# Optimization experiments

Hardware: AMD Instinct MI355X
Metric: run time of the kernel (lower is better)

The kernel has to match this reference:

```python
import jax, jax.numpy as jnp
import numpy as np

B, S, D = 4, 4096, 2048
K, H = 64, 32
HD = K // H  # 2
LN_EPS = 1e-5


def setup_inputs() -> dict:
    key = jax.random.key(0)
    ks = jax.random.split(key, 8)
    def xavier(k, shape):
        fan_in, fan_out = shape[1], shape[0]
        lim = float(np.sqrt(6.0 / (fan_in + fan_out)))
        return jax.random.uniform(k, shape, jnp.float32, -lim, lim)
    return {
        "x": jax.random.normal(ks[0], (B, S, D), jnp.float32),
        "norm_w": jnp.ones((D,), jnp.float32),
        "norm_b": jnp.zeros((D,), jnp.float32),
        "qkv_w": xavier(ks[1], (3 * K, D)),
        "qkv_b": jnp.zeros((3 * K,), jnp.float32),
        "fm_w": xavier(ks[2], (HD, HD)),
        "fm_b": jnp.zeros((HD,), jnp.float32),
        "out_w": xavier(ks[3], (D, K)),
        "out_b": jnp.zeros((D,), jnp.float32),
    }


def reference(x, norm_w, norm_b, qkv_w, qkv_b, fm_w, fm_b, out_w, out_b):
    # LayerNorm
    mu = jnp.mean(x, axis=-1, keepdims=True)
    var = jnp.var(x, axis=-1, keepdims=True)
    xn = (x - mu) * jax.lax.rsqrt(var + LN_EPS) * norm_w + norm_b
    # QKV projection: [B,S,3K]
    qkv = xn @ qkv_w.T + qkv_b
    q, k, v = jnp.split(qkv, 3, axis=-1)
    # [B,S,K] -> [B,H,S,hd]
    def heads(t):
        return t.reshape(B, S, H, HD).transpose(0, 2, 1, 3)
    q, k, v = heads(q), heads(k), heads(v)
    # feature map: ReLU(Linear)
    q = jax.nn.relu(q @ fm_w.T + fm_b)
    k = jax.nn.relu(k @ fm_w.T + fm_b)
    # linear attention: kv state [B,H,hd,hd]
    kv = jnp.einsum('bhsd,bhse->bhde', k, v)
    attn = jnp.einsum('bhsd,bhde->bhse', q, kv)
    k_sum = jnp.sum(k, axis=2)                      # [B,H,hd]
    q_k_sum = jnp.einsum('bhsd,bhd->bhs', q, k_sum)[..., None]
    attn = attn / (q_k_sum + 1e-8)
    # merge heads -> [B,S,K]
    attn = attn.transpose(0, 2, 1, 3).reshape(B, S, K)
    out = attn @ out_w.T + out_b
    return x + out
```

## Files before the change

### kernel.cpp

```cpp
#include <hip/hip_runtime.h>
#include <hip/hip_bf16.h>
#include <stdint.h>

typedef unsigned short ushort_t;

#define BB 4
#define SS 4096
#define DD 2048
#define KKC 64
#define HH 32
#define NT (BB*SS)
#define NQKV 192
#define QB 64

typedef float f32x4 __attribute__((ext_vector_type(4)));
typedef short s16x8 __attribute__((ext_vector_type(8)));

__device__ __forceinline__ ushort_t f2bf(float f) {
    union { float f; uint32_t u; } c; c.f = f;
    uint32_t u = c.u + 0x7fffu + ((c.u >> 16) & 1u);
    return (ushort_t)(u >> 16);
}
__device__ __forceinline__ float bf2f(ushort_t b) {
    union { uint32_t u; float f; } c; c.u = (uint32_t)b << 16; return c.f;
}

__device__ __forceinline__ uint32_t cvtpk(float lo, float hi) {
    uint32_t r;
    asm("v_cvt_pk_bf16_f32 %0, %1, %2" : "=v"(r) : "v"(lo), "v"(hi));
    return r;
}

__device__ __forceinline__ void mfma16(f32x4& d, s16x8 a, s16x8 b) {
    asm volatile("v_mfma_f32_16x16x32_bf16 %0, %1, %2, %0" : "+v"(d) : "v"(a), "v"(b));
}

__global__ __launch_bounds__(256) void k_pre(
    const float* __restrict__ qkv_w, const float* __restrict__ nw,
    const float* __restrict__ nb, const float* __restrict__ qkv_b,
    const float* __restrict__ out_w,
    ushort_t* __restrict__ W1, ushort_t* __restrict__ W2,
    float* __restrict__ S, float* __restrict__ qb2) {
    int bid = blockIdx.x;
    if (bid < 256) {
        int E = bid * 256 + threadIdx.x;
        if (E < 49152) {
            int lane = E & 63; int rest = E >> 6;
            int f = rest % 12, g = rest / 12;
            int col = f * 16 + (lane & 15);
            int k0 = g * 32 + 8 * (lane >> 4);
            const float* src = qkv_w + (size_t)col * DD + k0;
            const float* wp = nw + k0;
            union { ushort_t u[8]; uint4 v; } cv;
            #pragma unroll
            for (int e = 0; e < 8; ++e) cv.u[e] = f2bf(src[e] * wp[e]);
            *(uint4*)(W1 + (size_t)E * 8) = cv.v;
        } else {
            int E2 = E - 49152;
            int lane = E2 & 63; int rest = E2 >> 6;
            int kk = rest & 1, F = rest >> 1;
            int n = F * 16 + (lane & 15);
            int k0 = kk * 32 + 8 * (lane >> 4);
            const float* src = out_w + (size_t)n * KKC + k0;
            union { ushort_t u[8]; uint4 v; } cv;
            #pragma unroll
            for (int e = 0; e < 8; ++e) cv.u[e] = f2bf(src[e]);
            *(uint4*)(W2 + (size_t)E2 * 8) = cv.v;
        }
    } else {
        int col = (bid - 256) * 4 + (threadIdx.x >> 6);
        int lane = threadIdx.x & 63;
        float s = 0.f, qb = 0.f;
        for (int j = 0; j < 32; ++j) {
            int k = j * 64 + lane;
            float w = qkv_w[(size_t)col * DD + k];
            s += bf2f(f2bf(w * nw[k]));
            qb += nb[k] * w;
        }
        #pragma unroll
        for (int off = 32; off >= 1; off >>= 1) {
            s += __shfl_xor(s, off);
            qb += __shfl_xor(qb, off);
        }
        if (lane == 0) { S[col] = s; qb2[col] = qb + qkv_b[col]; }
    }
}

__global__ __launch_bounds__(512, 2) void k_qkv(
    const float* __restrict__ x, const ushort_t* __restrict__ W1,
    const float* __restrict__ S, const float* __restrict__ qb2,
    const float* __restrict__ fm_w, const float* __restrict__ fm_b,
    float* __restrict__ qfeat,
    float* __restrict__ kvpart)
{
    __shared__ __align__(16) union {
        ushort_t xb[8][2][16][64];
        float cep[QB][NQKV];
    } sm;
    __shared__ float kvred[32][16][6];
    __shared__ float stats[QB][2];

    const int tid = threadIdx.x;
    const int wave = tid >> 6, lane = tid & 63;
    const int rg = wave & 3, ch = wave >> 2;
    const int m0 = blockIdx.x * QB;
    const int fbase = ch * 6;
    const int l15 = lane & 15, q4 = lane >> 4;
    const bool doStats = (ch == 0);

    const float* xbase = x + (size_t)(m0 + rg * 16 + q4) * DD + l15 * 4;
    int wb[4];
    #pragma unroll
    for (int i = 0; i < 4; ++i) {
        int r = i * 4 + q4;
        wb[i] = r * 128 + ((l15 >> 1) ^ (r & 7)) * 16 + (l15 & 1) * 8;
    }
    const s16x8* __restrict__ Wp = (const s16x8*)W1;

    f32x4 acc[6];
    #pragma unroll
    for (int j = 0; j < 6; ++j) acc[j] = (f32x4){0.f, 0.f, 0.f, 0.f};
    float st1[4] = {0.f, 0.f, 0.f, 0.f}, st2[4] = {0.f, 0.f, 0.f, 0.f};

#define LOADX(T, X) do { \
        _Pragma("unroll") \
        for (int i_ = 0; i_ < 4; ++i_) \
            X[i_] = *(const float4*)(xbase + (size_t)(i_ * 4) * DD + (T) * 64); \
    } while (0)

#define LOADB(T, D) do { \
        _Pragma("unroll") \
        for (int kb_ = 0; kb_ < 2; ++kb_) \
        { _Pragma("unroll") \
          for (int cf_ = 0; cf_ < 6; ++cf_) \
            D[kb_][cf_] = Wp[((size_t)(2 * (T) + kb_) * 12 + fbase + cf_) * 64 + lane]; } \
    } while (0)

#define CVTW(T, X) do { \
        char* xbw_ = (char*)&sm.xb[wave][(T) & 1][0][0]; \
        _Pragma("unroll") \
        for (int i_ = 0; i_ < 4; ++i_) { \
            if (doStats) { \
                st1[i_] += X[i_].x + X[i_].y + X[i_].z + X[i_].w; \
                st2[i_] += X[i_].x*X[i_].x + X[i_].y*X[i_].y \
                         + X[i_].z*X[i_].z + X[i_].w*X[i_].w; \
            } \
            uint2 w_; \
            w_.x = cvtpk(X[i_].x, X[i_].y); \
            w_.y = cvtpk(X[i_].z, X[i_].w); \
            *(uint2*)(xbw_ + wb[i_]) = w_; \
        } \
    } while (0)

#define AREAD(T, AF) do { \
        const char* xbr_ = (const char*)&sm.xb[wave][(T) & 1][0][0]; \
        _Pragma("unroll") \
        for (int kb_ = 0; kb_ < 2; ++kb_) \
            AF[kb_] = *(const s16x8*)(xbr_ + l15 * 128 + (((kb_ * 4 + q4) ^ (l15 & 7)) << 4)); \
    } while (0)

#define MM(AF, D) do { \
        _Pragma("unroll") \
        for (int kb_ = 0; kb_ < 2; ++kb_) \
        { _Pragma("unroll") \
          for (int cf_ = 0; cf_ < 6; ++cf_) \
            mfma16(acc[cf_], AF[kb_], D[kb_][cf_]); } \
    } while (0)

    float4 xA[4], xB[4];
    s16x8 Ba[2][6], Bb[2][6], af[2];

    LOADX(0, xA);
    LOADB(0, Ba);
    CVTW(0, xA);

    for (int tp = 0; tp < 16; ++tp) {
        const int t0 = 2 * tp, t1 = t0 + 1;
        LOADX(t1, xB); LOADB(t1, Bb);
        AREAD(t0, af); MM(af, Ba);
        CVTW(t1, xB);
        if (t1 < 31) { LOADX(t1 + 1, xA); LOADB(t1 + 1, Ba); }
        AREAD(t1, af); MM(af, Bb);
        if (t1 < 31) CVTW(t1 + 1, xA);
    }
#undef LOADX
#undef LOADB
#undef CVTW
#undef AREAD
#undef MM

    if (doStats) {
        #pragma unroll
        for (int i = 0; i < 4; ++i) {
            float s1 = st1[i], s2 = st2[i];
            s1 += __shfl_xor(s1, 1); s2 += __shfl_xor(s2, 1);
            s1 += __shfl_xor(s1, 2); s2 += __shfl_xor(s2, 2);
            s1 += __shfl_xor(s1, 4); s2 += __shfl_xor(s2, 4);
            s1 += __shfl_xor(s1, 8); s2 += __shfl_xor(s2, 8);
            if (l15 == 0) {
                int row = rg * 16 + i * 4 + q4;
                float mu = s1 * (1.f / DD);
                float var = s2 * (1.f / DD) - mu * mu;
                stats[row][0] = mu;
                stats[row][1] = rsqrtf(var + 1e-5f);
            }
        }
    }
    __syncthreads();

    #pragma unroll
    for (int j = 0; j < 6; ++j) {
        int col = (fbase + j) * 16 + l15;
        int rbase = rg * 16 + q4 * 4;
        #pragma unroll
        for (int r = 0; r < 4; ++r)
            sm.cep[rbase + r][col] = acc[j][r];
    }
    __syncthreads();

    const int h = tid & 31, gg = tid >> 5;
    const float fm00 = fm_w[0], fm01 = fm_w[1], fm10 = fm_w[2], fm11 = fm_w[3];
    const float fb0 = fm_b[0], fb1 = fm_b[1];
    const float Sq0 = S[2*h],      Sq1 = S[2*h+1],      cq0 = qb2[2*h],      cq1 = qb2[2*h+1];
    const float Sk0 = S[64+2*h],   Sk1 = S[64+2*h+1],   ck0 = qb2[64+2*h],   ck1 = qb2[64+2*h+1];
    const float Sv0 = S[128+2*h],  Sv1 = S[128+2*h+1],  cv0 = qb2[128+2*h],  cv1 = qb2[128+2*h+1];
    float kv00=0, kv01=0, kv10=0, kv11=0, ks0=0, ks1=0;
    #pragma unroll
    for (int i = 0; i < 4; ++i) {
        int tt = gg * 4 + i;
        float mu = stats[tt][0], rs = stats[tt][1];
        float f = mu * rs;
        float q0 = rs * sm.cep[tt][2*h]      - f * Sq0 + cq0;
        float q1 = rs * sm.cep[tt][2*h+1]    - f * Sq1 + cq1;
        float k0 = rs * sm.cep[tt][64+2*h]   - f * Sk0 + ck0;
        float k1 = rs * sm.cep[tt][64+2*h+1] - f * Sk1 + ck1;
        float v0 = rs * sm.cep[tt][128+2*h]  - f * Sv0 + cv0;
        float v1 = rs * sm.cep[tt][128+2*h+1]- f * Sv1 + cv1;
        float qp0 = fmaxf(fm00*q0 + fm01*q1 + fb0, 0.f);
        float qp1 = fmaxf(fm10*q0 + fm11*q1 + fb1, 0.f);
        float kp0 = fmaxf(fm00*k0 + fm01*k1 + fb0, 0.f);
        float kp1 = fmaxf(fm10*k0 + fm11*k1 + fb1, 0.f);
        *(float2*)(qfeat + (size_t)(m0 + tt) * KKC + 2*h) = make_float2(qp0, qp1);
        kv00 += kp0*v0; kv01 += kp0*v1; kv10 += kp1*v0; kv11 += kp1*v1;
        ks0 += kp0; ks1 += kp1;
    }
    kvred[h][gg][0]=kv00; kvred[h][gg][1]=kv01; kvred[h][gg][2]=kv10;
    kvred[h][gg][3]=kv11; kvred[h][gg][4]=ks0;  kvred[h][gg][5]=ks1;
    __syncthreads();
    if (tid < 192) {
        int h2 = tid / 6, j = tid % 6;
        float s = 0.f;
        #pragma unroll
        for (int g2 = 0; g2 < 16; ++g2) s += kvred[h2][g2][j];
        kvpart[(size_t)blockIdx.x * 192 + tid] = s;
    }
}

#define CEP_STRIDE 260
__global__ __launch_bounds__(512, 4) void k_out(
    const float* __restrict__ qfeat, const float* __restrict__ kvpart,
    const ushort_t* __restrict__ W2, const float* __restrict__ out_b,
    const float* __restrict__ x, float* __restrict__ out) {
    __shared__ float skv[192];
    __shared__ __align__(16) float cep[32 * CEP_STRIDE];
    const int tid = threadIdx.x, wave = tid >> 6, lane = tid & 63;
    const int rg = wave & 1, cq = wave >> 1;
    const int mb = blockIdx.x >> 1, nb = blockIdx.x & 1;
    const int m0 = mb * 32;
    const int n0 = nb * 1024;
    const int b = m0 >> 12;

    if (tid < 192) {
        float s = 0.f;
        #pragma unroll 8
        for (int j = 0; j < 64; ++j)
            s += kvpart[(size_t)(b * 64 + j) * 192 + tid];
        skv[tid] = s;
    }

    const int arow = m0 + rg * 16 + (lane & 15);
    const int ksub = 8 * (lane >> 4);
    float4 qa0 = *(const float4*)(qfeat + (size_t)arow * KKC + ksub);
    float4 qa1 = *(const float4*)(qfeat + (size_t)arow * KKC + ksub + 4);
    float4 qb0 = *(const float4*)(qfeat + (size_t)arow * KKC + 32 + ksub);
    float4 qb1 = *(const float4*)(qfeat + (size_t)arow * KKC + 32 + ksub + 4);
    __syncthreads();

    union { ushort_t u[8]; s16x8 v; } ca, cb;
    {
        float qs[8] = {qa0.x,qa0.y,qa0.z,qa0.w,qa1.x,qa1.y,qa1.z,qa1.w};
        float rs[8] = {qb0.x,qb0.y,qb0.z,qb0.w,qb1.x,qb1.y,qb1.z,qb1.w};
        #pragma unroll
        for (int e = 0; e < 8; e += 2) {
            int h = (ksub + e) >> 1;
            const float* kv = skv + h * 6;
            float q0 = qs[e], q1 = qs[e+1];
            float inv = 1.f / (q0 * kv[4] + q1 * kv[5] + 1e-8f);
            ca.u[e]   = f2bf((q0 * kv[0] + q1 * kv[2]) * inv);
            ca.u[e+1] = f2bf((q0 * kv[1] + q1 * kv[3]) * inv);
            const float* kw = skv + (h + 16) * 6;
            float p0 = rs[e], p1 = rs[e+1];
            float iw = 1.f / (p0 * kw[4] + p1 * kw[5] + 1e-8f);
            cb.u[e]   = f2bf((p0 * kw[0] + p1 * kw[2]) * iw);
            cb.u[e+1] = f2bf((p0 * kw[1] + p1 * kw[3]) * iw);
        }
    }

    f32x4 acc[16];
    #pragma unroll
    for (int j = 0; j < 16; ++j) acc[j] = (f32x4){0.f, 0.f, 0.f, 0.f};
    #pragma unroll
    for (int j = 0; j < 16; ++j) {
        int Fg = (n0 >> 4) + cq + 4 * j;
        s16x8 b0 = *(const s16x8*)(W2 + ((size_t)(Fg * 2 + 0) * 64 + lane) * 8);
        s16x8 b1 = *(const s16x8*)(W2 + ((size_t)(Fg * 2 + 1) * 64 + lane) * 8);
        mfma16(acc[j], ca.v, b0);
        mfma16(acc[j], cb.v, b1);
    }

    const int wrow = rg * 16 + 4 * (lane >> 4);
    #pragma unroll
    for (int n = 0; n < 4; ++n) {
        #pragma unroll
        for (int i = 0; i < 4; ++i) {
            int col = cq * 16 + i * 64 + (lane & 15);
            #pragma unroll
            for (int r = 0; r < 4; ++r)
                cep[(wrow + r) * CEP_STRIDE + col] = acc[4 * n + i][r];
        }
        __syncthreads();
        #pragma unroll
        for (int p = 0; p < 4; ++p) {
            int row = p * 8 + (tid >> 6);
            int c4 = tid & 63;
            float4 c = *(const float4*)(cep + row * CEP_STRIDE + c4 * 4);
            int gcol = n0 + n * 256 + c4 * 4;
            size_t off = (size_t)(m0 + row) * DD + gcol;
            float4 xr = *(const float4*)(x + off);
            float4 ob = *(const float4*)(out_b + gcol);
            float4 o;
            o.x = c.x + ob.x + xr.x; o.y = c.y + ob.y + xr.y;
            o.z = c.z + ob.z + xr.z; o.w = c.w + ob.w + xr.w;
            *(float4*)(out + off) = o;
        }
        __syncthreads();
    }
}

extern "C" void kernel_launch(void* const* d_in, const int* in_sizes, int n_in,
                              void* d_out, int out_size, void* d_ws, size_t ws_size,
                              hipStream_t stream) {
    const float* x     = (const float*)d_in[0];
    const float* nw    = (const float*)d_in[1];
    const float* nb    = (const float*)d_in[2];
    const float* qkv_w = (const float*)d_in[3];
    const float* qkv_b = (const float*)d_in[4];
    const float* fm_w  = (const float*)d_in[5];
    const float* fm_b  = (const float*)d_in[6];
    const float* out_w = (const float*)d_in[7];
    const float* out_b = (const float*)d_in[8];
    float* out = (float*)d_out;

    char* ws = (char*)d_ws;
    ushort_t* W1 = (ushort_t*)ws;     ws += (size_t)NQKV * DD * 2;
    ushort_t* W2 = (ushort_t*)ws;     ws += (size_t)DD * KKC * 2;
    float* qfeat = (float*)ws;        ws += (size_t)NT * KKC * 4;
    float* kvpart = (float*)ws;       ws += (size_t)256 * 192 * 4;
    float* Svec = (float*)ws;         ws += (size_t)NQKV * 4;
    float* qb2 = (float*)ws;          ws += (size_t)NQKV * 4;

    k_pre<<<304, 256, 0, stream>>>(qkv_w, nw, nb, qkv_b, out_w, W1, W2, Svec, qb2);
    k_qkv<<<NT / QB, 512, 0, stream>>>(x, W1, Svec, qb2, fm_w, fm_b, qfeat, kvpart);
    k_out<<<(NT / 32) * 2, 512, 0, stream>>>(qfeat, kvpart, W2, out_b, x, out);
}
```

Before: 121.2 us.

## Stage QKV weights via global_load_lds with BK=128 double buffering; add kv reduce kernel

The QKV GEMM main loop is restructured. The block loads a 64x128 x tile cooperatively and converts it to bf16 into swizzled LDS. The pre-packed W1 tiles are staged straight into LDS with global_load_lds, double-buffered, using explicit waitcnt/barrier control and setprio around the MFMAs. Each wave now computes 32 rows by 3 column fragments instead of 16 rows by 6, so B operands are shared through LDS rather than loaded per wave from global. Separately, a tiny k_red kernel reduces the kvpart sums once, so every k_out block no longer repeats the 64-way reduction. This adds one kernel launch and larger LDS usage, which may lower occupancy.

After: 119.3 us. Within noise of the previous version (-1.6%).

```diff
diff --git a/kernel.cpp b/kernel.cpp
--- a/kernel.cpp
+++ b/kernel.cpp
@@ -12,6 +12,7 @@
 #define NT (BB*SS)
 #define NQKV 192
 #define QB 64
+#define BK 128
 
 typedef float f32x4 __attribute__((ext_vector_type(4)));
 typedef short s16x8 __attribute__((ext_vector_type(8)));
@@ -33,6 +34,13 @@
 
 __device__ __forceinline__ void mfma16(f32x4& d, s16x8 a, s16x8 b) {
     asm volatile("v_mfma_f32_16x16x32_bf16 %0, %1, %2, %0" : "+v"(d) : "v"(a), "v"(b));
+}
+
+__device__ __forceinline__ void gload_lds16(const void* gsrc, void* ldst) {
+    __builtin_amdgcn_global_load_lds(
+        (const __attribute__((address_space(1))) unsigned int*)gsrc,
+        (__attribute__((address_space(3))) unsigned int*)ldst,
+        16, 0, 0);
 }
 
 __global__ __launch_bounds__(256) void k_pre(
@@ -94,7 +102,12 @@
     float* __restrict__ kvpart)
 {
     __shared__ __align__(16) union {
-        ushort_t xb[8][2][16][64];
+        struct {
+            ushort_t B0[3072 * 8];
+            ushort_t X0[QB * BK];
+            ushort_t B1[3072 * 8];
+            ushort_t X1[QB * BK];
+        } s;
         float cep[QB][NQKV];
     } sm;
     __shared__ float kvred[32][16][6];
@@ -102,119 +115,137 @@
 
     const int tid = threadIdx.x;
     const int wave = tid >> 6, lane = tid & 63;
-    const int rg = wave & 3, ch = wave >> 2;
+    const int rg = wave & 1, ch = wave >> 1;
     const int m0 = blockIdx.x * QB;
-    const int fbase = ch * 6;
     const int l15 = lane & 15, q4 = lane >> 4;
-    const bool doStats = (ch == 0);
-
-    const float* xbase = x + (size_t)(m0 + rg * 16 + q4) * DD + l15 * 4;
-    int wb[4];
-    #pragma unroll
-    for (int i = 0; i < 4; ++i) {
-        int r = i * 4 + q4;
-        wb[i] = r * 128 + ((l15 >> 1) ^ (r & 7)) * 16 + (l15 & 1) * 8;
-    }
-    const s16x8* __restrict__ Wp = (const s16x8*)W1;
-
-    f32x4 acc[6];
-    #pragma unroll
-    for (int j = 0; j < 6; ++j) acc[j] = (f32x4){0.f, 0.f, 0.f, 0.f};
-    float st1[4] = {0.f, 0.f, 0.f, 0.f}, st2[4] = {0.f, 0.f, 0.f, 0.f};
-
-#define LOADX(T, X) do { \
+
+    const int row0 = tid >> 4;
+    const int sl0 = tid & 15;
+    const int row1 = row0 + 32;
+    const float* xs0 = x + (size_t)(m0 + row0) * DD + sl0 * 8;
+    const float* xs1 = x + (size_t)(m0 + row1) * DD + sl0 * 8;
+    const int wb0 = row0 * 256 + ((sl0 ^ (row0 & 7)) << 4);
+    const int wb1 = row1 * 256 + ((sl0 ^ (row1 & 7)) << 4);
+
+    f32x4 acc[2][3];
+    #pragma unroll
+    for (int rf = 0; rf < 2; ++rf)
+        #pragma unroll
+        for (int f = 0; f < 3; ++f) acc[rf][f] = (f32x4){0.f, 0.f, 0.f, 0.f};
+    float st1[2] = {0.f, 0.f}, st2[2] = {0.f, 0.f};
+
+    float4 xa[4];
+
+#define XISSUE(T) do { \
+        xa[0] = *(const float4*)(xs0 + (size_t)(T) * BK); \
+        xa[1] = *(const float4*)(xs0 + (size_t)(T) * BK + 4); \
+        xa[2] = *(const float4*)(xs1 + (size_t)(T) * BK); \
+        xa[3] = *(const float4*)(xs1 + (size_t)(T) * BK + 4); \
+    } while (0)
+
+#define BSTAGE(T, BARR) do { \
         _Pragma("unroll") \
-        for (int i_ = 0; i_ < 4; ++i_) \
-            X[i_] = *(const float4*)(xbase + (size_t)(i_ * 4) * DD + (T) * 64); \
-    } while (0)
-
-#define LOADB(T, D) do { \
-        _Pragma("unroll") \
-        for (int kb_ = 0; kb_ < 2; ++kb_) \
-        { _Pragma("unroll") \
-          for (int cf_ = 0; cf_ < 6; ++cf_) \
-            D[kb_][cf_] = Wp[((size_t)(2 * (T) + kb_) * 12 + fbase + cf_) * 64 + lane]; } \
-    } while (0)
-
-#define CVTW(T, X) do { \
-        char* xbw_ = (char*)&sm.xb[wave][(T) & 1][0][0]; \
-        _Pragma("unroll") \
-        for (int i_ = 0; i_ < 4; ++i_) { \
-            if (doStats) { \
-                st1[i_] += X[i_].x + X[i_].y + X[i_].z + X[i_].w; \
-                st2[i_] += X[i_].x*X[i_].x + X[i_].y*X[i_].y \
-                         + X[i_].z*X[i_].z + X[i_].w*X[i_].w; \
-            } \
-            uint2 w_; \
-            w_.x = cvtpk(X[i_].x, X[i_].y); \
-            w_.y = cvtpk(X[i_].z, X[i_].w); \
-            *(uint2*)(xbw_ + wb[i_]) = w_; \
+        for (int i_ = 0; i_ < 6; ++i_) { \
+            int eb_ = i_ * 512 + wave * 64; \
+            gload_lds16((const char*)W1 + ((size_t)(T) * 3072 + eb_ + lane) * 16, \
+                        (char*)(BARR) + eb_ * 16); \
         } \
     } while (0)
 
-#define AREAD(T, AF) do { \
-        const char* xbr_ = (const char*)&sm.xb[wave][(T) & 1][0][0]; \
+#define CVTW(XARR) do { \
+        st1[0] += xa[0].x+xa[0].y+xa[0].z+xa[0].w + xa[1].x+xa[1].y+xa[1].z+xa[1].w; \
+        st2[0] += xa[0].x*xa[0].x+xa[0].y*xa[0].y+xa[0].z*xa[0].z+xa[0].w*xa[0].w \
+                + xa[1].x*xa[1].x+xa[1].y*xa[1].y+xa[1].z*xa[1].z+xa[1].w*xa[1].w; \
+        st1[1] += xa[2].x+xa[2].y+xa[2].z+xa[2].w + xa[3].x+xa[3].y+xa[3].z+xa[3].w; \
+        st2[1] += xa[2].x*xa[2].x+xa[2].y*xa[2].y+xa[2].z*xa[2].z+xa[2].w*xa[2].w \
+                + xa[3].x*xa[3].x+xa[3].y*xa[3].y+xa[3].z*xa[3].z+xa[3].w*xa[3].w; \
+        uint4 w0_, w1_; \
+        w0_.x = cvtpk(xa[0].x, xa[0].y); w0_.y = cvtpk(xa[0].z, xa[0].w); \
+        w0_.z = cvtpk(xa[1].x, xa[1].y); w0_.w = cvtpk(xa[1].z, xa[1].w); \
+        w1_.x = cvtpk(xa[2].x, xa[2].y); w1_.y = cvtpk(xa[2].z, xa[2].w); \
+        w1_.z = cvtpk(xa[3].x, xa[3].y); w1_.w = cvtpk(xa[3].z, xa[3].w); \
+        *(uint4*)((char*)(XARR) + wb0) = w0_; \
+        *(uint4*)((char*)(XARR) + wb1) = w1_; \
+    } while (0)
+
+#define STEP_BODY(BARR, XARR) do { \
+        const char* bp_ = (const char*)(BARR); \
+        const char* xp_ = (const char*)(XARR); \
+        const int r0_ = rg * 32 + l15, r1_ = r0_ + 16; \
         _Pragma("unroll") \
-        for (int kb_ = 0; kb_ < 2; ++kb_) \
-            AF[kb_] = *(const s16x8*)(xbr_ + l15 * 128 + (((kb_ * 4 + q4) ^ (l15 & 7)) << 4)); \
+        for (int kb_ = 0; kb_ < 4; ++kb_) { \
+            s16x8 a0_ = *(const s16x8*)(xp_ + r0_ * 256 + (((kb_ * 4 + q4) ^ (r0_ & 7)) << 4)); \
+            s16x8 a1_ = *(const s16x8*)(xp_ + r1_ * 256 + (((kb_ * 4 + q4) ^ (r1_ & 7)) << 4)); \
+            __builtin_amdgcn_s_setprio(1); \
+            _Pragma("unroll") \
+            for (int f_ = 0; f_ < 3; ++f_) { \
+                s16x8 b_ = *(const s16x8*)(bp_ + ((kb_ * 12 + ch * 3 + f_) * 64 + lane) * 16); \
+                mfma16(acc[0][f_], a0_, b_); \
+                mfma16(acc[1][f_], a1_, b_); \
+            } \
+            __builtin_amdgcn_s_setprio(0); \
+        } \
     } while (0)
 
-#define MM(AF, D) do { \
-        _Pragma("unroll") \
-        for (int kb_ = 0; kb_ < 2; ++kb_) \
-        { _Pragma("unroll") \
-          for (int cf_ = 0; cf_ < 6; ++cf_) \
-            mfma16(acc[cf_], AF[kb_], D[kb_][cf_]); } \
+#define WAITN(N) asm volatile("s_waitcnt vmcnt(" #N ")" ::: "memory")
+#define LGKM0()  asm volatile("s_waitcnt lgkmcnt(0)" ::: "memory")
+#define BARR_()  do { __builtin_amdgcn_s_barrier(); __builtin_amdgcn_sched_barrier(0); } while (0)
+
+#define ITER(T, CB, CX, NB_, NX_) do { \
+        XISSUE((T) + 1); \
+        BSTAGE((T) + 1, NB_); \
+        STEP_BODY(CB, CX); \
+        WAITN(6); \
+        CVTW(NX_); \
+        LGKM0(); \
+        WAITN(0); \
+        BARR_(); \
     } while (0)
 
-    float4 xA[4], xB[4];
-    s16x8 Ba[2][6], Bb[2][6], af[2];
-
-    LOADX(0, xA);
-    LOADB(0, Ba);
-    CVTW(0, xA);
-
-    for (int tp = 0; tp < 16; ++tp) {
-        const int t0 = 2 * tp, t1 = t0 + 1;
-        LOADX(t1, xB); LOADB(t1, Bb);
-        AREAD(t0, af); MM(af, Ba);
-        CVTW(t1, xB);
-        if (t1 < 31) { LOADX(t1 + 1, xA); LOADB(t1 + 1, Ba); }
-        AREAD(t1, af); MM(af, Bb);
-        if (t1 < 31) CVTW(t1 + 1, xA);
-    }
-#undef LOADX
-#undef LOADB
-#undef CVTW
-#undef AREAD
-#undef MM
-
-    if (doStats) {
-        #pragma unroll
-        for (int i = 0; i < 4; ++i) {
-            float s1 = st1[i], s2 = st2[i];
-            s1 += __shfl_xor(s1, 1); s2 += __shfl_xor(s2, 1);
-            s1 += __shfl_xor(s1, 2); s2 += __shfl_xor(s2, 2);
-            s1 += __shfl_xor(s1, 4); s2 += __shfl_xor(s2, 4);
-            s1 += __shfl_xor(s1, 8); s2 += __shfl_xor(s2, 8);
-            if (l15 == 0) {
-                int row = rg * 16 + i * 4 + q4;
-                float mu = s1 * (1.f / DD);
-                float var = s2 * (1.f / DD) - mu * mu;
-                stats[row][0] = mu;
-                stats[row][1] = rsqrtf(var + 1e-5f);
-            }
-        }
-    }
-    __syncthreads();
-
-    #pragma unroll
-    for (int j = 0; j < 6; ++j) {
-        int col = (fbase + j) * 16 + l15;
-        int rbase = rg * 16 + q4 * 4;
-        #pragma unroll
-        for (int r = 0; r < 4; ++r)
-            sm.cep[rbase + r][col] = acc[j][r];
+    XISSUE(0);
+    BSTAGE(0, sm.s.B0);
+    WAITN(6);
+    CVTW(sm.s.X0);
+    LGKM0();
+    WAITN(0);
+    BARR_();
+
+    #pragma unroll
+    for (int tp = 0; tp < 7; ++tp) {
+        ITER(2 * tp,     sm.s.B0, sm.s.X0, sm.s.B1, sm.s.X1);
+        ITER(2 * tp + 1, sm.s.B1, sm.s.X1, sm.s.B0, sm.s.X0);
+    }
+    ITER(14, sm.s.B0, sm.s.X0, sm.s.B1, sm.s.X1);
+    STEP_BODY(sm.s.B1, sm.s.X1);
+
+    #pragma unroll
+    for (int j = 0; j < 2; ++j) {
+        st1[j] += __shfl_xor(st1[j], 1); st2[j] += __shfl_xor(st2[j], 1);
+        st1[j] += __shfl_xor(st1[j], 2); st2[j] += __shfl_xor(st2[j], 2);
+        st1[j] += __shfl_xor(st1[j], 4); st2[j] += __shfl_xor(st2[j], 4);
+        st1[j] += __shfl_xor(st1[j], 8); st2[j] += __shfl_xor(st2[j], 8);
+    }
+    if (l15 == 0) {
+        #pragma unroll
+        for (int j = 0; j < 2; ++j) {
+            int row = wave * 4 + q4 + j * 32;
+            float mu = st1[j] * (1.f / DD);
+            float var = st2[j] * (1.f / DD) - mu * mu;
+            stats[row][0] = mu;
+            stats[row][1] = rsqrtf(var + 1e-5f);
+        }
+    }
+
+    #pragma unroll
+    for (int rf = 0; rf < 2; ++rf) {
+        int rbase = rg * 32 + rf * 16 + q4 * 4;
+        #pragma unroll
+        for (int f = 0; f < 3; ++f) {
+            int col = (ch * 3 + f) * 16 + l15;
+            #pragma unroll
+            for (int r = 0; r < 4; ++r)
+                sm.cep[rbase + r][col] = acc[rf][f][r];
+        }
     }
     __syncthreads();
 
@@ -254,11 +285,29 @@
         for (int g2 = 0; g2 < 16; ++g2) s += kvred[h2][g2][j];
         kvpart[(size_t)blockIdx.x * 192 + tid] = s;
     }
+#undef XISSUE
+#undef BSTAGE
+#undef CVTW
+#undef STEP_BODY
+#undef WAITN
+#undef LGKM0
+#undef BARR_
+#undef ITER
+}
+
+__global__ void k_red(const float* __restrict__ kvpart, float* __restrict__ kvstate) {
+    int idx = blockIdx.x * 256 + threadIdx.x;
+    if (idx >= BB * HH * 6) return;
+    int b = idx / 192, r = idx % 192;
+    float s = 0.f;
+    for (int blk = 0; blk < 64; ++blk)
+        s += kvpart[(size_t)(b * 64 + blk) * 192 + r];
+    kvstate[idx] = s;
 }
 
 #define CEP_STRIDE 260
 __global__ __launch_bounds__(512, 4) void k_out(
-    const float* __restrict__ qfeat, const float* __restrict__ kvpart,
+    const float* __restrict__ qfeat, const float* __restrict__ kvstate,
     const ushort_t* __restrict__ W2, const float* __restrict__ out_b,
     const float* __restrict__ x, float* __restrict__ out) {
     __shared__ float skv[192];
@@ -269,14 +318,7 @@
     const int m0 = mb * 32;
     const int n0 = nb * 1024;
     const int b = m0 >> 12;
-
-    if (tid < 192) {
-        float s = 0.f;
-        #pragma unroll 8
-        for (int j = 0; j < 64; ++j)
-            s += kvpart[(size_t)(b * 64 + j) * 192 + tid];
-        skv[tid] = s;
-    }
+    if (tid < 192) skv[tid] = kvstate[b * 192 + tid];
 
     const int arow = m0 + rg * 16 + (lane & 15);
     const int ksub = 8 * (lane >> 4);
@@ -366,10 +408,12 @@
     ushort_t* W2 = (ushort_t*)ws;     ws += (size_t)DD * KKC * 2;
     float* qfeat = (float*)ws;        ws += (size_t)NT * KKC * 4;
     float* kvpart = (float*)ws;       ws += (size_t)256 * 192 * 4;
+    float* kvstate = (float*)ws;      ws += (size_t)BB * HH * 6 * 4;
     float* Svec = (float*)ws;         ws += (size_t)NQKV * 4;
     float* qb2 = (float*)ws;          ws += (size_t)NQKV * 4;
 
     k_pre<<<304, 256, 0, stream>>>(qkv_w, nw, nb, qkv_b, out_w, W1, W2, Svec, qb2);
     k_qkv<<<NT / QB, 512, 0, stream>>>(x, W1, Svec, qb2, fm_w, fm_b, qfeat, kvpart);
-    k_out<<<(NT / 32) * 2, 512, 0, stream>>>(qfeat, kvpart, W2, out_b, x, out);
-}
+    k_red<<<3, 256, 0, stream>>>(kvpart, kvstate);
+    k_out<<<(NT / 32) * 2, 512, 0, stream>>>(qfeat, kvstate, W2, out_b, x, out);
+}
```
